# Performance work log

Measured on AMD Instinct MI355X. Metric: run time of the kernel, lower is better.

Reference implementation:

```python
import jax, jax.numpy as jnp
import numpy as np

B, S, H = 4, 2048, 1024
N_EXPERTS = 8
EXPERT_DIM = 1024  # must equal H (see module: wo features = expert_dim, output added to zeros_like(x))
TOP_K = 2
Z_LOSS_COEF = 0.001


def setup_inputs() -> dict:
    key = jax.random.key(0)
    ks = jax.random.split(key, 8)
    s_h = 1.0 / np.sqrt(H)
    s_e = 1.0 / np.sqrt(EXPERT_DIM)
    return {
        "x": jax.random.normal(ks[0], (B, S, H), dtype=jnp.float32),
        "router_w": jax.random.normal(ks[1], (H, N_EXPERTS), dtype=jnp.float32) * s_h,
        "router_b": jnp.zeros((N_EXPERTS,), dtype=jnp.float32),
        "wi_w": jax.random.normal(ks[2], (N_EXPERTS, H, EXPERT_DIM), dtype=jnp.float32) * s_h,
        "wi_b": jnp.zeros((N_EXPERTS, EXPERT_DIM), dtype=jnp.float32),
        "wo_w": jax.random.normal(ks[3], (N_EXPERTS, EXPERT_DIM, EXPERT_DIM), dtype=jnp.float32) * s_e,
        "wo_b": jnp.zeros((N_EXPERTS, EXPERT_DIM), dtype=jnp.float32),
    }


def reference(x, router_w, router_b, wi_w, wi_b, wo_w, wo_b):
    # Router (deterministic=True: no jitter noise, no dropout)
    logits = jnp.einsum("bsh,he->bse", x, router_w) + router_b        # [B,S,Ne]
    probs = jax.nn.softmax(logits, axis=-1)
    z_loss = jnp.mean(jnp.square(jax.nn.logsumexp(logits, axis=-1))) * Z_LOSS_COEF
    topk_p, topk_i = jax.lax.top_k(probs, TOP_K)                      # [B,S,2]
    topk_p = topk_p / jnp.sum(topk_p, axis=-1, keepdims=True)
    # Faithful to source: mask[...,None] ([B,S,2,1]) broadcasts against x ([B,S,H])
    # producing [B,S,2,H]; combined output has that shape.
    out = jnp.zeros((B, S, TOP_K, H), dtype=x.dtype)
    n_experts = wi_w.shape[0]
    for e in range(n_experts):  # fixed small expert loop, as in source
        mask = (topk_i == e)                                          # [B,S,2]
        p = jnp.where(mask, topk_p, 0.0)                              # [B,S,2]
        xin = jnp.where(mask[..., None], x[:, :, None, :], 0.0)       # [B,S,2,H]
        h = jax.nn.gelu(jnp.einsum("bskh,hd->bskd", xin, wi_w[e]) + wi_b[e])
        y = jnp.einsum("bskd,do->bsko", h, wo_w[e]) + wo_b[e]         # [B,S,2,H]
        out = out + y * p[..., None]
    return out, z_loss
```

## Files before the change

kernel.cpp:

```cpp
#include <hip/hip_runtime.h>

typedef unsigned short u16;
typedef unsigned int   u32;
typedef __bf16 bf16x8 __attribute__((ext_vector_type(8)));
typedef float  f32x4  __attribute__((ext_vector_type(4)));

#define NTOK   8192
#define NSLOT  16384

#define XB_OFF   0UL
#define WIT_OFF  16777216UL
#define WOT_OFF  33554432UL
#define HB_OFF   50331648UL
#define RE_OFF   83886080UL
#define RP_OFF   83951616UL
#define SEG_OFF  84017152UL
#define META_OFF 84082688UL
#define WS_NEED  (META_OFF + 2048UL)

__device__ __forceinline__ u16 f2b(float f) {
  u32 u = __float_as_uint(f);
  u32 r = (u + 0x7fffu + ((u >> 16) & 1u)) >> 16;
  return (u16)r;
}

__device__ __forceinline__ void async_cp16(const void* g, void* l) {
  __builtin_amdgcn_global_load_lds(
      (const __attribute__((address_space(1))) u32*)g,
      (__attribute__((address_space(3))) u32*)l, 16, 0, 0);
}

__device__ __forceinline__ float gelu_f(float v) {
  float u  = 0.7978845608028654f * (v + 0.044715f * v * v * v);
  float ex = __expf(2.0f * u);
  float th = 1.0f - 2.0f / (ex + 1.0f);
  return 0.5f * v * (1.0f + th);
}

__global__ __launch_bounds__(256) void k_transpose(const float* __restrict__ wi,
                                                   const float* __restrict__ wo,
                                                   u16* __restrict__ wit,
                                                   u16* __restrict__ wot) {
  __shared__ float t[64][65];
  int z = blockIdx.z;
  int e = z & 7;
  const float* src = ((z < 8) ? wi : wo) + ((size_t)e << 20);
  u16* dst = ((z < 8) ? wit : wot) + ((size_t)e << 20);
  int h0 = blockIdx.y * 64, d0 = blockIdx.x * 64;
  int tid = threadIdx.x;
#pragma unroll
  for (int j = 0; j < 4; j++) {
    int f = tid + 256 * j;
    int r = f >> 4, c4 = f & 15;
    float4 v = *(const float4*)&src[(size_t)(h0 + r) * 1024 + d0 + c4 * 4];
    t[r][c4 * 4 + 0] = v.x; t[r][c4 * 4 + 1] = v.y;
    t[r][c4 * 4 + 2] = v.z; t[r][c4 * 4 + 3] = v.w;
  }
  __syncthreads();
#pragma unroll
  for (int j = 0; j < 4; j++) {
    int f = tid + 256 * j;
    int d = f >> 4, c4 = f & 15;
    u32 p0 = (u32)f2b(t[c4 * 4 + 0][d]) | ((u32)f2b(t[c4 * 4 + 1][d]) << 16);
    u32 p1 = (u32)f2b(t[c4 * 4 + 2][d]) | ((u32)f2b(t[c4 * 4 + 3][d]) << 16);
    u32* dp = (u32*)&dst[(size_t)(d0 + d) * 1024 + h0 + c4 * 4];
    dp[0] = p0; dp[1] = p1;
  }
}

__global__ __launch_bounds__(256) void k_router(const float* __restrict__ x,
    const float* __restrict__ rw, const float* __restrict__ rb,
    u16* __restrict__ xb, int* __restrict__ route_e, float* __restrict__ route_p,
    int* __restrict__ counts, float* __restrict__ zsum) {
  __shared__ float lx[32][257];
  __shared__ float lrw[1024 * 9];
  __shared__ float llog[32 * 9];
  int tid = threadIdx.x;
  int t0  = blockIdx.x * 32;
#pragma unroll
  for (int j = 0; j < 8; j++) {
    int f = tid + 256 * j;
    int h = f >> 1, half = f & 1;
    float4 v = *(const float4*)&rw[h * 8 + half * 4];
    lrw[h * 9 + half * 4 + 0] = v.x; lrw[h * 9 + half * 4 + 1] = v.y;
    lrw[h * 9 + half * 4 + 2] = v.z; lrw[h * 9 + half * 4 + 3] = v.w;
  }
  int tl = tid & 31, e = tid >> 5;
  float acc = rb[e];
  for (int ch = 0; ch < 4; ch++) {
    __syncthreads();
#pragma unroll
    for (int j = 0; j < 8; j++) {
      int f = tid + 256 * j;
      int r = f >> 6, c4 = f & 63;
      float4 v = *(const float4*)&x[(size_t)(t0 + r) * 1024 + ch * 256 + c4 * 4];
      lx[r][c4 * 4 + 0] = v.x; lx[r][c4 * 4 + 1] = v.y;
      lx[r][c4 * 4 + 2] = v.z; lx[r][c4 * 4 + 3] = v.w;
    }
    __syncthreads();
    for (int hl = 0; hl < 256; hl++)
      acc += lx[tl][hl] * lrw[(ch * 256 + hl) * 9 + e];
#pragma unroll
    for (int j = 0; j < 16; j++) {
      int f = tid + 256 * j;
      int r = f >> 7, cp = f & 127;
      u32 pk = (u32)f2b(lx[r][cp * 2]) | ((u32)f2b(lx[r][cp * 2 + 1]) << 16);
      *(u32*)&xb[(size_t)(t0 + r) * 1024 + ch * 256 + cp * 2] = pk;
    }
  }
  llog[tl * 9 + e] = acc;
  __syncthreads();
  if (tid < 32) {
    int t = t0 + tid;
    float lg[8];
#pragma unroll
    for (int k = 0; k < 8; k++) lg[k] = llog[tid * 9 + k];
    int e0 = 0; float b0 = lg[0];
#pragma unroll
    for (int k = 1; k < 8; k++) if (lg[k] > b0) { b0 = lg[k]; e0 = k; }
    int e1 = -1; float b1 = -3.4e38f;
#pragma unroll
    for (int k = 0; k < 8; k++) { if (k == e0) continue; if (lg[k] > b1) { b1 = lg[k]; e1 = k; } }
    float s = 0.f;
#pragma unroll
    for (int k = 0; k < 8; k++) s += __expf(lg[k] - b0);
    float lse = b0 + __logf(s);
    float z = lse * lse;
    float q1 = __expf(b1 - b0);
    float r0 = 1.0f / (1.0f + q1);
    route_e[t * 2 + 0] = e0; route_e[t * 2 + 1] = e1;
    route_p[t * 2 + 0] = r0; route_p[t * 2 + 1] = q1 / (1.0f + q1);
    atomicAdd(&counts[e0], 1); atomicAdd(&counts[e1], 1);
    for (int off = 16; off; off >>= 1) z += __shfl_down(z, off, 32);
    if (tid == 0) atomicAdd(zsum, z);
  }
}

__global__ void k_scan(int* __restrict__ counts, int* __restrict__ offs,
                       int* __restrict__ cursors, int* __restrict__ ntiles,
                       int* __restrict__ tile_e, int* __restrict__ tile_r0,
                       const float* __restrict__ zsum, float* __restrict__ zout) {
  int o = 0, nt = 0;
  offs[0] = 0;
  for (int e = 0; e < 8; e++) {
    int c = counts[e];
    cursors[e] = o;
    for (int r = 0; r < c; r += 320) { tile_e[nt] = e; tile_r0[nt] = o + r; nt++; }
    o += c;
    offs[e + 1] = o;
  }
  *ntiles = nt;
  *zout = *zsum * (0.001f / 8192.0f);
}

__global__ __launch_bounds__(256) void k_scatter(const int* __restrict__ route_e,
                                                 int* __restrict__ cursors,
                                                 int* __restrict__ seg) {
  int i = blockIdx.x * 256 + threadIdx.x;
  int e = route_e[i];
  int lane = threadIdx.x & 63;
#pragma unroll
  for (int ex = 0; ex < 8; ex++) {
    unsigned long long mask = __ballot(e == ex);
    if (e == ex) {
      int cnt = __popcll(mask);
      int leader = __ffsll((long long)mask) - 1;
      int base = 0;
      if (lane == leader) base = atomicAdd(&cursors[ex], cnt);
      base = __shfl(base, leader, 64);
      int rank = __popcll(mask & ((1ull << lane) - 1ull));
      seg[base + rank] = i;
    }
  }
}


#define BAR()    asm volatile("s_barrier" ::: "memory")
#define WAITV0() asm volatile("s_waitcnt vmcnt(0)" ::: "memory")

#define STAGE_A(B, KT, J) async_cp16(asrc[J] + (KT) * 64, &As[B][(w * 40 + (J) * 8) * 64])
#define STAGE_B(B, KT, J) async_cp16(bsrc[J] + (KT) * 64, &Bs[B][(w * 32 + (J) * 8) * 64])

#define PHASE(CUR, Q)                                                              \
  do {                                                                             \
    bf16x8 af[2][2], bfr[2][4];                                                    \
    _Pragma("unroll")                                                              \
    for (int kk = 0; kk < 2; kk++) {                                               \
      int c = ((kk * 4 + rh) ^ (rl & 7)) * 8;                                      \
      _Pragma("unroll")                                                            \
      for (int d = 0; d < 2; d++)                                                  \
        af[kk][d] = *(const bf16x8*)&As[CUR][(wr * 160 + (2 * (Q) + d) * 16 + rl) * 64 + c]; \
      _Pragma("unroll")                                                            \
      for (int n = 0; n < 4; n++)                                                  \
        bfr[kk][n] = *(const bf16x8*)&Bs[CUR][(wc * 64 + n * 16 + rl) * 64 + c];   \
    }                                                                              \
    __builtin_amdgcn_s_setprio(1);                                                 \
    _Pragma("unroll")                                                              \
    for (int kk = 0; kk < 2; kk++)                                                 \
      _Pragma("unroll")                                                            \
      for (int d = 0; d < 2; d++)                                                  \
        _Pragma("unroll")                                                          \
        for (int n = 0; n < 4; n++)                                                \
          acc[2 * (Q) + d][n] = __builtin_amdgcn_mfma_f32_16x16x32_bf16(           \
              af[kk][d], bfr[kk][n], acc[2 * (Q) + d][n], 0, 0, 0);                \
    __builtin_amdgcn_s_setprio(0);                                                 \
  } while (0)

#define GEMM_BODY()                                                                \
  _Pragma("unroll")                                                                \
  for (int j = 0; j < 5; j++) STAGE_A(0, 0, j);                                    \
  _Pragma("unroll")                                                                \
  for (int j = 0; j < 4; j++) STAGE_B(0, 0, j);                                    \
  WAITV0(); BAR();                                                                 \
  _Pragma("unroll 2")                                                              \
  for (int g = 0; g < 16; g++) {                                                   \
    int cur = g & 1, nxt = cur ^ 1;                                                \
    bool pf = (g < 15);                                                            \
    if (pf) { STAGE_A(nxt, g + 1, 0); STAGE_A(nxt, g + 1, 1); STAGE_A(nxt, g + 1, 2); \
              STAGE_B(nxt, g + 1, 0); STAGE_B(nxt, g + 1, 1); }                    \
    PHASE(cur, 0); BAR();                                                          \
    if (pf) { STAGE_A(nxt, g + 1, 3); STAGE_A(nxt, g + 1, 4);                      \
              STAGE_B(nxt, g + 1, 2); STAGE_B(nxt, g + 1, 3); }                    \
    PHASE(cur, 1); BAR();                                                          \
    PHASE(cur, 2); BAR();                                                          \
    PHASE(cur, 3); BAR();                                                          \
    PHASE(cur, 4);                                                                 \
    WAITV0(); BAR();                                                               \
  }

__global__ __launch_bounds__(512, 2) void k_gemm_h(
    const u16* __restrict__ xb, const u16* __restrict__ wit, const float* __restrict__ wib,
    u16* __restrict__ hb, const int* __restrict__ seg, const int* __restrict__ offs,
    const int* __restrict__ tile_e, const int* __restrict__ tile_r0,
    const int* __restrict__ ntiles) {
  __shared__ u16 As[2][320 * 64];
  __shared__ u16 Bs[2][256 * 64];
  int bid = blockIdx.x;
  int swz = (bid & 7) * 30 + (bid >> 3);
  int mt = swz >> 2;
  if (mt >= *ntiles) return;
  int n0 = (swz & 3) << 8;
  int e = tile_e[mt], r0 = tile_r0[mt], end = offs[e + 1];
  int tid = threadIdx.x;
  int w = tid >> 6, l = tid & 63;
  int lr = l >> 3, lc = l & 7;
  int cs = lc ^ lr;
  const u16* asrc[5];
  const u16* bsrc[4];
#pragma unroll
  for (int j = 0; j < 5; j++) {
    int gr = r0 + w * 40 + j * 8 + lr;
    int idx = seg[(gr < end) ? gr : r0];
    asrc[j] = xb + (size_t)(idx >> 1) * 1024 + cs * 8;
  }
#pragma unroll
  for (int j = 0; j < 4; j++)
    bsrc[j] = wit + ((size_t)e << 20) + (size_t)(n0 + w * 32 + j * 8 + lr) * 1024 + cs * 8;
  f32x4 acc[10][4];
  f32x4 z4 = {0.f, 0.f, 0.f, 0.f};
#pragma unroll
  for (int m = 0; m < 10; m++)
#pragma unroll
    for (int n = 0; n < 4; n++) acc[m][n] = z4;
  int wr = w >> 2, wc = w & 3;
  int rl = l & 15, rh = l >> 4;
  GEMM_BODY()
#pragma unroll
  for (int n = 0; n < 4; n++) {
    int col = n0 + wc * 64 + n * 16 + rl;
    float bias = wib[e * 1024 + col];
#pragma unroll
    for (int m = 0; m < 10; m++) {
      int rbase = r0 + wr * 160 + m * 16 + rh * 4;
#pragma unroll
      for (int j = 0; j < 4; j++) {
        int gr = rbase + j;
        if (gr < end)
          hb[(size_t)gr * 1024 + col] = f2b(gelu_f(acc[m][n][j] + bias));
      }
    }
  }
}

__global__ __launch_bounds__(512, 2) void k_gemm_o(
    const u16* __restrict__ hb, const u16* __restrict__ wot, const float* __restrict__ wob,
    float* __restrict__ out, const int* __restrict__ seg, const int* __restrict__ offs,
    const int* __restrict__ tile_e, const int* __restrict__ tile_r0,
    const int* __restrict__ ntiles, const float* __restrict__ route_p) {
  __shared__ u16 As[2][320 * 64];
  __shared__ u16 Bs[2][256 * 64];
  int bid = blockIdx.x;
  int swz = (bid & 7) * 30 + (bid >> 3);
  int mt = swz >> 2;
  if (mt >= *ntiles) return;
  int n0 = (swz & 3) << 8;
  int e = tile_e[mt], r0 = tile_r0[mt], end = offs[e + 1];
  int tid = threadIdx.x;
  int w = tid >> 6, l = tid & 63;
  int lr = l >> 3, lc = l & 7;
  int cs = lc ^ lr;
  const u16* asrc[5];
  const u16* bsrc[4];
#pragma unroll
  for (int j = 0; j < 5; j++) {
    int gr = r0 + w * 40 + j * 8 + lr;
    int grc = (gr < end) ? gr : r0;
    asrc[j] = hb + (size_t)grc * 1024 + cs * 8;
  }
#pragma unroll
  for (int j = 0; j < 4; j++)
    bsrc[j] = wot + ((size_t)e << 20) + (size_t)(n0 + w * 32 + j * 8 + lr) * 1024 + cs * 8;
  f32x4 acc[10][4];
  f32x4 z4 = {0.f, 0.f, 0.f, 0.f};
#pragma unroll
  for (int m = 0; m < 10; m++)
#pragma unroll
    for (int n = 0; n < 4; n++) acc[m][n] = z4;
  int wr = w >> 2, wc = w & 3;
  int rl = l & 15, rh = l >> 4;
  GEMM_BODY()
#pragma unroll
  for (int m = 0; m < 10; m++) {
    int rbase = r0 + wr * 160 + m * 16 + rh * 4;
#pragma unroll
    for (int j = 0; j < 4; j++) {
      int gr = rbase + j;
      if (gr >= end) continue;
      int idx = seg[gr];
      float p = route_p[idx];
      float* orow = out + (size_t)idx * 1024;
#pragma unroll
      for (int n = 0; n < 4; n++) {
        int col = n0 + wc * 64 + n * 16 + rl;
        orow[col] = (acc[m][n][j] + wob[e * 1024 + col]) * p;
      }
    }
  }
}

extern "C" void kernel_launch(void* const* d_in, const int* in_sizes, int n_in,
                              void* d_out, int out_size, void* d_ws, size_t ws_size,
                              hipStream_t stream) {
  if (ws_size < WS_NEED) return;
  const float* x   = (const float*)d_in[0];
  const float* rw  = (const float*)d_in[1];
  const float* rb  = (const float*)d_in[2];
  const float* wiw = (const float*)d_in[3];
  const float* wib = (const float*)d_in[4];
  const float* wow = (const float*)d_in[5];
  const float* wob = (const float*)d_in[6];
  float* out = (float*)d_out;
  char* ws = (char*)d_ws;

  u16*   xb      = (u16*)(ws + XB_OFF);
  u16*   wit     = (u16*)(ws + WIT_OFF);
  u16*   wot     = (u16*)(ws + WOT_OFF);
  u16*   hb      = (u16*)(ws + HB_OFF);
  int*   route_e = (int*)(ws + RE_OFF);
  float* route_p = (float*)(ws + RP_OFF);
  int*   seg     = (int*)(ws + SEG_OFF);
  int*   counts  = (int*)(ws + META_OFF + 0);
  int*   offs    = (int*)(ws + META_OFF + 64);
  int*   cursors = (int*)(ws + META_OFF + 128);
  int*   ntiles  = (int*)(ws + META_OFF + 192);
  float* zsum    = (float*)(ws + META_OFF + 196);
  int*   tile_e  = (int*)(ws + META_OFF + 256);
  int*   tile_r0 = (int*)(ws + META_OFF + 1024);

  hipMemsetAsync(ws + META_OFF, 0, 256, stream);
  k_transpose<<<dim3(16, 16, 16), 256, 0, stream>>>(wiw, wow, wit, wot);
  k_router<<<256, 256, 0, stream>>>(x, rw, rb, xb, route_e, route_p, counts, zsum);
  k_scan<<<1, 1, 0, stream>>>(counts, offs, cursors, ntiles, tile_e, tile_r0,
                              zsum, out + (out_size - 1));
  k_scatter<<<64, 256, 0, stream>>>(route_e, cursors, seg);
  k_gemm_h<<<240, 512, 0, stream>>>(xb, wit, wib, hb, seg, offs,
                                    tile_e, tile_r0, ntiles);
  k_gemm_o<<<240, 512, 0, stream>>>(hb, wot, wob, out, seg, offs,
                                    tile_e, tile_r0, ntiles, route_p);
}
```

Before: 270.5 us.

## Use one wavefront per token in router and restructure GEMM k-loop staging

The router moves from a 32-tokens-per-block LDS design to one wavefront per token. Each wavefront reads the row directly, writes the bf16 copy, and reduces the 8 logits with xor shuffles. The z-loss becomes a per-token buffer that the scan kernel sums with 256 threads, replacing a single global atomic. The GEMM main loop now issues all prefetches for the next k-tile up front and computes the whole 10x4 MFMA tile per kk, with one barrier per k-tile instead of five phases each separated by a barrier. This trades fewer barriers for more live registers and less interleaving of loads with MFMAs.

```diff
diff --git a/kernel.cpp b/kernel.cpp
--- a/kernel.cpp
+++ b/kernel.cpp
@@ -16,7 +16,8 @@
 #define RP_OFF   83951616UL
 #define SEG_OFF  84017152UL
 #define META_OFF 84082688UL
-#define WS_NEED  (META_OFF + 2048UL)
+#define ZB_OFF   (META_OFF + 4096UL)
+#define WS_NEED  (ZB_OFF + 32768UL)
 
 __device__ __forceinline__ u16 f2b(float f) {
   u32 u = __float_as_uint(f);
@@ -71,50 +72,36 @@
 __global__ __launch_bounds__(256) void k_router(const float* __restrict__ x,
     const float* __restrict__ rw, const float* __restrict__ rb,
     u16* __restrict__ xb, int* __restrict__ route_e, float* __restrict__ route_p,
-    int* __restrict__ counts, float* __restrict__ zsum) {
-  __shared__ float lx[32][257];
-  __shared__ float lrw[1024 * 9];
-  __shared__ float llog[32 * 9];
-  int tid = threadIdx.x;
-  int t0  = blockIdx.x * 32;
-#pragma unroll
-  for (int j = 0; j < 8; j++) {
-    int f = tid + 256 * j;
-    int h = f >> 1, half = f & 1;
-    float4 v = *(const float4*)&rw[h * 8 + half * 4];
-    lrw[h * 9 + half * 4 + 0] = v.x; lrw[h * 9 + half * 4 + 1] = v.y;
-    lrw[h * 9 + half * 4 + 2] = v.z; lrw[h * 9 + half * 4 + 3] = v.w;
-  }
-  int tl = tid & 31, e = tid >> 5;
-  float acc = rb[e];
-  for (int ch = 0; ch < 4; ch++) {
-    __syncthreads();
-#pragma unroll
-    for (int j = 0; j < 8; j++) {
-      int f = tid + 256 * j;
-      int r = f >> 6, c4 = f & 63;
-      float4 v = *(const float4*)&x[(size_t)(t0 + r) * 1024 + ch * 256 + c4 * 4];
-      lx[r][c4 * 4 + 0] = v.x; lx[r][c4 * 4 + 1] = v.y;
-      lx[r][c4 * 4 + 2] = v.z; lx[r][c4 * 4 + 3] = v.w;
-    }
-    __syncthreads();
-    for (int hl = 0; hl < 256; hl++)
-      acc += lx[tl][hl] * lrw[(ch * 256 + hl) * 9 + e];
-#pragma unroll
-    for (int j = 0; j < 16; j++) {
-      int f = tid + 256 * j;
-      int r = f >> 7, cp = f & 127;
-      u32 pk = (u32)f2b(lx[r][cp * 2]) | ((u32)f2b(lx[r][cp * 2 + 1]) << 16);
-      *(u32*)&xb[(size_t)(t0 + r) * 1024 + ch * 256 + cp * 2] = pk;
-    }
-  }
-  llog[tl * 9 + e] = acc;
-  __syncthreads();
-  if (tid < 32) {
-    int t = t0 + tid;
-    float lg[8];
-#pragma unroll
-    for (int k = 0; k < 8; k++) lg[k] = llog[tid * 9 + k];
+    int* __restrict__ counts, float* __restrict__ zbuf) {
+  int wid = (blockIdx.x * 256 + threadIdx.x) >> 6;
+  int l = threadIdx.x & 63;
+  const float* xr = x + (size_t)wid * 1024 + l * 16;
+  float4 xv[4];
+#pragma unroll
+  for (int j = 0; j < 4; j++) xv[j] = *(const float4*)(xr + j * 4);
+  const float* xf = (const float*)xv;
+  u32* xbp = (u32*)(((u16*)xb) + (size_t)wid * 1024 + l * 16);
+#pragma unroll
+  for (int j = 0; j < 8; j++)
+    xbp[j] = (u32)f2b(xf[2 * j]) | ((u32)f2b(xf[2 * j + 1]) << 16);
+  float a0 = 0, a1 = 0, a2 = 0, a3 = 0, a4 = 0, a5 = 0, a6 = 0, a7 = 0;
+  const float* rwp = rw + (size_t)l * 128;
+#pragma unroll
+  for (int j = 0; j < 16; j++) {
+    float xj = xf[j];
+    float4 w0 = *(const float4*)(rwp + j * 8);
+    float4 w1 = *(const float4*)(rwp + j * 8 + 4);
+    a0 += xj * w0.x; a1 += xj * w0.y; a2 += xj * w0.z; a3 += xj * w0.w;
+    a4 += xj * w1.x; a5 += xj * w1.y; a6 += xj * w1.z; a7 += xj * w1.w;
+  }
+  float lg[8] = {a0, a1, a2, a3, a4, a5, a6, a7};
+#pragma unroll
+  for (int e = 0; e < 8; e++)
+#pragma unroll
+    for (int off = 32; off; off >>= 1) lg[e] += __shfl_xor(lg[e], off, 64);
+  if (l == 0) {
+#pragma unroll
+    for (int e = 0; e < 8; e++) lg[e] += rb[e];
     int e0 = 0; float b0 = lg[0];
 #pragma unroll
     for (int k = 1; k < 8; k++) if (lg[k] > b0) { b0 = lg[k]; e0 = k; }
@@ -125,32 +112,41 @@
 #pragma unroll
     for (int k = 0; k < 8; k++) s += __expf(lg[k] - b0);
     float lse = b0 + __logf(s);
-    float z = lse * lse;
     float q1 = __expf(b1 - b0);
-    float r0 = 1.0f / (1.0f + q1);
-    route_e[t * 2 + 0] = e0; route_e[t * 2 + 1] = e1;
-    route_p[t * 2 + 0] = r0; route_p[t * 2 + 1] = q1 / (1.0f + q1);
+    route_e[wid * 2 + 0] = e0; route_e[wid * 2 + 1] = e1;
+    route_p[wid * 2 + 0] = 1.0f / (1.0f + q1);
+    route_p[wid * 2 + 1] = q1 / (1.0f + q1);
+    zbuf[wid] = lse * lse;
     atomicAdd(&counts[e0], 1); atomicAdd(&counts[e1], 1);
-    for (int off = 16; off; off >>= 1) z += __shfl_down(z, off, 32);
-    if (tid == 0) atomicAdd(zsum, z);
-  }
-}
-
-__global__ void k_scan(int* __restrict__ counts, int* __restrict__ offs,
-                       int* __restrict__ cursors, int* __restrict__ ntiles,
-                       int* __restrict__ tile_e, int* __restrict__ tile_r0,
-                       const float* __restrict__ zsum, float* __restrict__ zout) {
-  int o = 0, nt = 0;
-  offs[0] = 0;
-  for (int e = 0; e < 8; e++) {
-    int c = counts[e];
-    cursors[e] = o;
-    for (int r = 0; r < c; r += 320) { tile_e[nt] = e; tile_r0[nt] = o + r; nt++; }
-    o += c;
-    offs[e + 1] = o;
-  }
-  *ntiles = nt;
-  *zout = *zsum * (0.001f / 8192.0f);
+  }
+}
+
+__global__ __launch_bounds__(256) void k_scan(
+    const int* __restrict__ counts, int* __restrict__ offs,
+    int* __restrict__ cursors, int* __restrict__ ntiles,
+    int* __restrict__ tile_e, int* __restrict__ tile_r0,
+    const float* __restrict__ zbuf, float* __restrict__ zout) {
+  __shared__ float zs[4];
+  int tid = threadIdx.x;
+  float z = 0.f;
+  for (int i = tid; i < NTOK; i += 256) z += zbuf[i];
+#pragma unroll
+  for (int off = 32; off; off >>= 1) z += __shfl_xor(z, off, 64);
+  if ((tid & 63) == 0) zs[tid >> 6] = z;
+  __syncthreads();
+  if (tid == 0) {
+    *zout = (zs[0] + zs[1] + zs[2] + zs[3]) * (0.001f / 8192.0f);
+    int o = 0, nt = 0;
+    offs[0] = 0;
+    for (int e = 0; e < 8; e++) {
+      int c = counts[e];
+      cursors[e] = o;
+      for (int r = 0; r < c; r += 320) { tile_e[nt] = e; tile_r0[nt] = o + r; nt++; }
+      o += c;
+      offs[e + 1] = o;
+    }
+    *ntiles = nt;
+  }
 }
 
 __global__ __launch_bounds__(256) void k_scatter(const int* __restrict__ route_e,
@@ -181,51 +177,46 @@
 #define STAGE_A(B, KT, J) async_cp16(asrc[J] + (KT) * 64, &As[B][(w * 40 + (J) * 8) * 64])
 #define STAGE_B(B, KT, J) async_cp16(bsrc[J] + (KT) * 64, &Bs[B][(w * 32 + (J) * 8) * 64])
 
-#define PHASE(CUR, Q)                                                              \
+#define STAGE_ALL(B, KT)                                                 \
+  do {                                                                   \
+    STAGE_A(B, KT, 0); STAGE_A(B, KT, 1); STAGE_A(B, KT, 2);             \
+    STAGE_A(B, KT, 3); STAGE_A(B, KT, 4);                                \
+    STAGE_B(B, KT, 0); STAGE_B(B, KT, 1); STAGE_B(B, KT, 2);             \
+    STAGE_B(B, KT, 3);                                                   \
+  } while (0)
+
+#define KTILE(CUR, NXT, G, PF)                                                     \
   do {                                                                             \
-    bf16x8 af[2][2], bfr[2][4];                                                    \
+    if (PF) STAGE_ALL(NXT, (G) + 1);                                               \
     _Pragma("unroll")                                                              \
     for (int kk = 0; kk < 2; kk++) {                                               \
       int c = ((kk * 4 + rh) ^ (rl & 7)) * 8;                                      \
-      _Pragma("unroll")                                                            \
-      for (int d = 0; d < 2; d++)                                                  \
-        af[kk][d] = *(const bf16x8*)&As[CUR][(wr * 160 + (2 * (Q) + d) * 16 + rl) * 64 + c]; \
+      bf16x8 bfr[4], af[10];                                                       \
       _Pragma("unroll")                                                            \
       for (int n = 0; n < 4; n++)                                                  \
-        bfr[kk][n] = *(const bf16x8*)&Bs[CUR][(wc * 64 + n * 16 + rl) * 64 + c];   \
-    }                                                                              \
-    __builtin_amdgcn_s_setprio(1);                                                 \
-    _Pragma("unroll")                                                              \
-    for (int kk = 0; kk < 2; kk++)                                                 \
+        bfr[n] = *(const bf16x8*)&Bs[CUR][(wc * 64 + n * 16 + rl) * 64 + c];       \
       _Pragma("unroll")                                                            \
-      for (int d = 0; d < 2; d++)                                                  \
+      for (int m = 0; m < 10; m++)                                                 \
+        af[m] = *(const bf16x8*)&As[CUR][(wr * 160 + m * 16 + rl) * 64 + c];       \
+      __builtin_amdgcn_s_setprio(1);                                               \
+      _Pragma("unroll")                                                            \
+      for (int m = 0; m < 10; m++)                                                 \
         _Pragma("unroll")                                                          \
         for (int n = 0; n < 4; n++)                                                \
-          acc[2 * (Q) + d][n] = __builtin_amdgcn_mfma_f32_16x16x32_bf16(           \
-              af[kk][d], bfr[kk][n], acc[2 * (Q) + d][n], 0, 0, 0);                \
-    __builtin_amdgcn_s_setprio(0);                                                 \
+          acc[m][n] = __builtin_amdgcn_mfma_f32_16x16x32_bf16(af[m], bfr[n],       \
+                                                              acc[m][n], 0, 0, 0); \
+      __builtin_amdgcn_s_setprio(0);                                               \
+    }                                                                              \
+    WAITV0(); BAR();                                                               \
   } while (0)
 
 #define GEMM_BODY()                                                                \
-  _Pragma("unroll")                                                                \
-  for (int j = 0; j < 5; j++) STAGE_A(0, 0, j);                                    \
-  _Pragma("unroll")                                                                \
-  for (int j = 0; j < 4; j++) STAGE_B(0, 0, j);                                    \
+  STAGE_ALL(0, 0);                                                                 \
   WAITV0(); BAR();                                                                 \
-  _Pragma("unroll 2")                                                              \
-  for (int g = 0; g < 16; g++) {                                                   \
-    int cur = g & 1, nxt = cur ^ 1;                                                \
-    bool pf = (g < 15);                                                            \
-    if (pf) { STAGE_A(nxt, g + 1, 0); STAGE_A(nxt, g + 1, 1); STAGE_A(nxt, g + 1, 2); \
-              STAGE_B(nxt, g + 1, 0); STAGE_B(nxt, g + 1, 1); }                    \
-    PHASE(cur, 0); BAR();                                                          \
-    if (pf) { STAGE_A(nxt, g + 1, 3); STAGE_A(nxt, g + 1, 4);                      \
-              STAGE_B(nxt, g + 1, 2); STAGE_B(nxt, g + 1, 3); }                    \
-    PHASE(cur, 1); BAR();                                                          \
-    PHASE(cur, 2); BAR();                                                          \
-    PHASE(cur, 3); BAR();                                                          \
-    PHASE(cur, 4);                                                                 \
-    WAITV0(); BAR();                                                               \
+  _Pragma("unroll 1")                                                              \
+  for (int g = 0; g < 16; g += 2) {                                                \
+    KTILE(0, 1, g, true);                                                          \
+    KTILE(1, 0, g + 1, (g + 1) < 15);                                              \
   }
 
 __global__ __launch_bounds__(512, 2) void k_gemm_h(
@@ -363,15 +354,15 @@
   int*   offs    = (int*)(ws + META_OFF + 64);
   int*   cursors = (int*)(ws + META_OFF + 128);
   int*   ntiles  = (int*)(ws + META_OFF + 192);
-  float* zsum    = (float*)(ws + META_OFF + 196);
   int*   tile_e  = (int*)(ws + META_OFF + 256);
   int*   tile_r0 = (int*)(ws + META_OFF + 1024);
+  float* zbuf    = (float*)(ws + ZB_OFF);
 
   hipMemsetAsync(ws + META_OFF, 0, 256, stream);
   k_transpose<<<dim3(16, 16, 16), 256, 0, stream>>>(wiw, wow, wit, wot);
-  k_router<<<256, 256, 0, stream>>>(x, rw, rb, xb, route_e, route_p, counts, zsum);
-  k_scan<<<1, 1, 0, stream>>>(counts, offs, cursors, ntiles, tile_e, tile_r0,
-                              zsum, out + (out_size - 1));
+  k_router<<<2048, 256, 0, stream>>>(x, rw, rb, xb, route_e, route_p, counts, zbuf);
+  k_scan<<<1, 256, 0, stream>>>(counts, offs, cursors, ntiles, tile_e, tile_r0,
+                                zbuf, out + (out_size - 1));
   k_scatter<<<64, 256, 0, stream>>>(route_e, cursors, seg);
   k_gemm_h<<<240, 512, 0, stream>>>(xb, wit, wib, hb, seg, offs,
                                     tile_e, tile_r0, ntiles);
```

Result: slower. 483.7 us (+78.8%).

## Rewrite router as wave-per-token dot with shuffles; count experts in scan kernel

Applied to the files above, without the earlier changes.

The router kernel now assigns one wavefront per group of four tokens. Each lane reads the x row directly, accumulates eight expert logits in registers and reduces them with cross-lane shuffles, replacing the LDS-staged tile with its padded transposes and barriers. The global atomics for expert counts and z-loss are removed: per-token z values go to a buffer, and the scan kernel, now 256 threads wide, counts experts with shared atomics and reduces z before building the tile list. This also drops the memset. The cost is that the scan kernel does more serial work in one block, and the router writes bf16 x with 2-byte scalar stores.

```diff
diff --git a/kernel.cpp b/kernel.cpp
--- a/kernel.cpp
+++ b/kernel.cpp
@@ -16,7 +16,8 @@
 #define RP_OFF   83951616UL
 #define SEG_OFF  84017152UL
 #define META_OFF 84082688UL
-#define WS_NEED  (META_OFF + 2048UL)
+#define ZB_OFF   (META_OFF + 4096UL)
+#define WS_NEED  (ZB_OFF + 32768UL)
 
 __device__ __forceinline__ u16 f2b(float f) {
   u32 u = __float_as_uint(f);
@@ -71,86 +72,81 @@
 __global__ __launch_bounds__(256) void k_router(const float* __restrict__ x,
     const float* __restrict__ rw, const float* __restrict__ rb,
     u16* __restrict__ xb, int* __restrict__ route_e, float* __restrict__ route_p,
-    int* __restrict__ counts, float* __restrict__ zsum) {
-  __shared__ float lx[32][257];
-  __shared__ float lrw[1024 * 9];
-  __shared__ float llog[32 * 9];
+    float* __restrict__ zbuf) {
+  int wv = blockIdx.x * 4 + (threadIdx.x >> 6);
+  int l = threadIdx.x & 63;
+#pragma unroll 1
+  for (int t = 0; t < 4; t++) {
+    int tok = wv * 4 + t;
+    const float* xrow = x + (size_t)tok * 1024;
+    u16* xbrow = xb + (size_t)tok * 1024;
+    float a[8] = {0.f, 0.f, 0.f, 0.f, 0.f, 0.f, 0.f, 0.f};
+#pragma unroll
+    for (int j = 0; j < 16; j++) {
+      int c = j * 64 + l;
+      float xj = xrow[c];
+      xbrow[c] = f2b(xj);
+      float4 w0 = *(const float4*)&rw[c * 8];
+      float4 w1 = *(const float4*)&rw[c * 8 + 4];
+      a[0] += xj * w0.x; a[1] += xj * w0.y; a[2] += xj * w0.z; a[3] += xj * w0.w;
+      a[4] += xj * w1.x; a[5] += xj * w1.y; a[6] += xj * w1.z; a[7] += xj * w1.w;
+    }
+#pragma unroll
+    for (int e = 0; e < 8; e++)
+#pragma unroll
+      for (int off = 32; off; off >>= 1) a[e] += __shfl_xor(a[e], off, 64);
+    if (l == 0) {
+#pragma unroll
+      for (int e = 0; e < 8; e++) a[e] += rb[e];
+      int e0 = 0; float b0 = a[0];
+#pragma unroll
+      for (int k = 1; k < 8; k++) if (a[k] > b0) { b0 = a[k]; e0 = k; }
+      int e1 = -1; float b1 = -3.4e38f;
+#pragma unroll
+      for (int k = 0; k < 8; k++) { if (k == e0) continue; if (a[k] > b1) { b1 = a[k]; e1 = k; } }
+      float s = 0.f;
+#pragma unroll
+      for (int k = 0; k < 8; k++) s += __expf(a[k] - b0);
+      float lse = b0 + __logf(s);
+      float q1 = __expf(b1 - b0);
+      route_e[tok * 2 + 0] = e0; route_e[tok * 2 + 1] = e1;
+      route_p[tok * 2 + 0] = 1.0f / (1.0f + q1);
+      route_p[tok * 2 + 1] = q1 / (1.0f + q1);
+      zbuf[tok] = lse * lse;
+    }
+  }
+}
+
+__global__ __launch_bounds__(256) void k_scan(
+    const int* __restrict__ route_e, int* __restrict__ offs,
+    int* __restrict__ cursors, int* __restrict__ ntiles,
+    int* __restrict__ tile_e, int* __restrict__ tile_r0,
+    const float* __restrict__ zbuf, float* __restrict__ zout) {
+  __shared__ int cnt[8];
+  __shared__ float zs[4];
   int tid = threadIdx.x;
-  int t0  = blockIdx.x * 32;
-#pragma unroll
-  for (int j = 0; j < 8; j++) {
-    int f = tid + 256 * j;
-    int h = f >> 1, half = f & 1;
-    float4 v = *(const float4*)&rw[h * 8 + half * 4];
-    lrw[h * 9 + half * 4 + 0] = v.x; lrw[h * 9 + half * 4 + 1] = v.y;
-    lrw[h * 9 + half * 4 + 2] = v.z; lrw[h * 9 + half * 4 + 3] = v.w;
-  }
-  int tl = tid & 31, e = tid >> 5;
-  float acc = rb[e];
-  for (int ch = 0; ch < 4; ch++) {
-    __syncthreads();
-#pragma unroll
-    for (int j = 0; j < 8; j++) {
-      int f = tid + 256 * j;
-      int r = f >> 6, c4 = f & 63;
-      float4 v = *(const float4*)&x[(size_t)(t0 + r) * 1024 + ch * 256 + c4 * 4];
-      lx[r][c4 * 4 + 0] = v.x; lx[r][c4 * 4 + 1] = v.y;
-      lx[r][c4 * 4 + 2] = v.z; lx[r][c4 * 4 + 3] = v.w;
-    }
-    __syncthreads();
-    for (int hl = 0; hl < 256; hl++)
-      acc += lx[tl][hl] * lrw[(ch * 256 + hl) * 9 + e];
-#pragma unroll
-    for (int j = 0; j < 16; j++) {
-      int f = tid + 256 * j;
-      int r = f >> 7, cp = f & 127;
-      u32 pk = (u32)f2b(lx[r][cp * 2]) | ((u32)f2b(lx[r][cp * 2 + 1]) << 16);
-      *(u32*)&xb[(size_t)(t0 + r) * 1024 + ch * 256 + cp * 2] = pk;
-    }
-  }
-  llog[tl * 9 + e] = acc;
+  if (tid < 8) cnt[tid] = 0;
   __syncthreads();
-  if (tid < 32) {
-    int t = t0 + tid;
-    float lg[8];
-#pragma unroll
-    for (int k = 0; k < 8; k++) lg[k] = llog[tid * 9 + k];
-    int e0 = 0; float b0 = lg[0];
-#pragma unroll
-    for (int k = 1; k < 8; k++) if (lg[k] > b0) { b0 = lg[k]; e0 = k; }
-    int e1 = -1; float b1 = -3.4e38f;
-#pragma unroll
-    for (int k = 0; k < 8; k++) { if (k == e0) continue; if (lg[k] > b1) { b1 = lg[k]; e1 = k; } }
-    float s = 0.f;
-#pragma unroll
-    for (int k = 0; k < 8; k++) s += __expf(lg[k] - b0);
-    float lse = b0 + __logf(s);
-    float z = lse * lse;
-    float q1 = __expf(b1 - b0);
-    float r0 = 1.0f / (1.0f + q1);
-    route_e[t * 2 + 0] = e0; route_e[t * 2 + 1] = e1;
-    route_p[t * 2 + 0] = r0; route_p[t * 2 + 1] = q1 / (1.0f + q1);
-    atomicAdd(&counts[e0], 1); atomicAdd(&counts[e1], 1);
-    for (int off = 16; off; off >>= 1) z += __shfl_down(z, off, 32);
-    if (tid == 0) atomicAdd(zsum, z);
-  }
-}
-
-__global__ void k_scan(int* __restrict__ counts, int* __restrict__ offs,
-                       int* __restrict__ cursors, int* __restrict__ ntiles,
-                       int* __restrict__ tile_e, int* __restrict__ tile_r0,
-                       const float* __restrict__ zsum, float* __restrict__ zout) {
-  int o = 0, nt = 0;
-  offs[0] = 0;
-  for (int e = 0; e < 8; e++) {
-    int c = counts[e];
-    cursors[e] = o;
-    for (int r = 0; r < c; r += 320) { tile_e[nt] = e; tile_r0[nt] = o + r; nt++; }
-    o += c;
-    offs[e + 1] = o;
-  }
-  *ntiles = nt;
-  *zout = *zsum * (0.001f / 8192.0f);
+  for (int i = tid; i < NSLOT; i += 256) atomicAdd(&cnt[route_e[i]], 1);
+  float z = 0.f;
+  for (int i = tid; i < NTOK; i += 256) z += zbuf[i];
+#pragma unroll
+  for (int off = 32; off; off >>= 1) z += __shfl_xor(z, off, 64);
+  if ((tid & 63) == 0) zs[tid >> 6] = z;
+  __syncthreads();
+  if (tid == 0) {
+    *zout = (zs[0] + zs[1] + zs[2] + zs[3]) * (0.001f / 8192.0f);
+    int o = 0, nt = 0;
+    offs[0] = 0;
+    for (int e = 0; e < 8; e++) {
+      int c = cnt[e];
+      cursors[e] = o;
+      for (int r = 0; r < c; r += 320) { tile_e[nt] = e; tile_r0[nt] = o + r; nt++; }
+      o += c;
+      offs[e + 1] = o;
+    }
+    *ntiles = nt;
+  }
 }
 
 __global__ __launch_bounds__(256) void k_scatter(const int* __restrict__ route_e,
@@ -359,19 +355,17 @@
   int*   route_e = (int*)(ws + RE_OFF);
   float* route_p = (float*)(ws + RP_OFF);
   int*   seg     = (int*)(ws + SEG_OFF);
-  int*   counts  = (int*)(ws + META_OFF + 0);
   int*   offs    = (int*)(ws + META_OFF + 64);
   int*   cursors = (int*)(ws + META_OFF + 128);
   int*   ntiles  = (int*)(ws + META_OFF + 192);
-  float* zsum    = (float*)(ws + META_OFF + 196);
   int*   tile_e  = (int*)(ws + META_OFF + 256);
   int*   tile_r0 = (int*)(ws + META_OFF + 1024);
-
-  hipMemsetAsync(ws + META_OFF, 0, 256, stream);
+  float* zbuf    = (float*)(ws + ZB_OFF);
+
   k_transpose<<<dim3(16, 16, 16), 256, 0, stream>>>(wiw, wow, wit, wot);
-  k_router<<<256, 256, 0, stream>>>(x, rw, rb, xb, route_e, route_p, counts, zsum);
-  k_scan<<<1, 1, 0, stream>>>(counts, offs, cursors, ntiles, tile_e, tile_r0,
-                              zsum, out + (out_size - 1));
+  k_router<<<512, 256, 0, stream>>>(x, rw, rb, xb, route_e, route_p, zbuf);
+  k_scan<<<1, 256, 0, stream>>>(route_e, offs, cursors, ntiles, tile_e, tile_r0,
+                                zbuf, out + (out_size - 1));
   k_scatter<<<64, 256, 0, stream>>>(route_e, cursors, seg);
   k_gemm_h<<<240, 512, 0, stream>>>(xb, wit, wib, hb, seg, offs,
                                     tile_e, tile_r0, ntiles);
```

New measurement: 223.6 us. -17.3%, faster.
